# Optimization experiments

Hardware: AMD Instinct MI355X
Metric: run time of the kernel (lower is better)

Reference implementation:

```python
import jax, jax.numpy as jnp
import numpy as np
from jax import lax

B = 16384
D_MODEL = 84
N_EXPERTS = 2
TOP_K = 2
HIDDEN = 2048


def _conv(x, w, b):
    # x: [N,C,H,W], w: [O,I,kh,kw] (torch OIHW), VALID padding, stride 1
    y = lax.conv_general_dilated(x, w, (1, 1), 'VALID',
                                 dimension_numbers=('NCHW', 'OIHW', 'NCHW'))
    return y + b[None, :, None, None]


def _maxpool2(x):
    return lax.reduce_window(x, -jnp.inf, lax.max,
                             (1, 1, 2, 2), (1, 1, 2, 2), 'VALID')


def setup_inputs() -> dict:
    key = jax.random.key(0)
    ks = jax.random.split(key, 17)
    s = 0.05
    return {
        'x': jax.random.normal(ks[0], (B, 3, 32, 32), jnp.float32),
        'conv1_w': jax.random.normal(ks[1], (6, 3, 5, 5), jnp.float32) * s,
        'conv1_b': jax.random.normal(ks[2], (6,), jnp.float32) * s,
        'conv2_w': jax.random.normal(ks[3], (16, 6, 5, 5), jnp.float32) * s,
        'conv2_b': jax.random.normal(ks[4], (16,), jnp.float32) * s,
        'fc1_w': jax.random.normal(ks[5], (400, 120), jnp.float32) * s,
        'fc1_b': jax.random.normal(ks[6], (120,), jnp.float32) * s,
        'fc2_w': jax.random.normal(ks[7], (120, 84), jnp.float32) * s,
        'fc2_b': jax.random.normal(ks[8], (84,), jnp.float32) * s,
        'gate_w': jax.random.normal(ks[9], (D_MODEL, N_EXPERTS), jnp.float32) * s,
        'exp_w1': jax.random.normal(ks[10], (N_EXPERTS, D_MODEL, HIDDEN), jnp.float32) * s,
        'exp_b1': jax.random.normal(ks[11], (N_EXPERTS, HIDDEN), jnp.float32) * s,
        'exp_w2': jax.random.normal(ks[12], (N_EXPERTS, HIDDEN, D_MODEL), jnp.float32) * s,
        'exp_b2': jax.random.normal(ks[13], (N_EXPERTS, D_MODEL), jnp.float32) * s,
        'fc3_w': jax.random.normal(ks[14], (84, 10), jnp.float32) * s,
        'fc3_b': jax.random.normal(ks[15], (10,), jnp.float32) * s,
    }


def _moe(x, gate_w, exp_w1, exp_b1, exp_w2, exp_b2):
    # tutel top-k gate: softmax over expert logits, select top-k, renormalize
    n = x.shape[0]
    scores = jax.nn.softmax(x @ gate_w, axis=-1)          # [N,E]
    top_v, top_i = lax.top_k(scores, TOP_K)               # [N,k]
    gates = top_v / jnp.sum(top_v, axis=-1, keepdims=True)
    # dense combine weights [N,E] (zero where not routed)
    comb = jnp.zeros((n, N_EXPERTS), x.dtype).at[
        jnp.arange(n)[:, None], top_i].set(gates)
    # grouped expert FFN (E=2: evaluate both, weight-combine)
    h = jax.nn.relu(jnp.einsum('nd,edh->enh', x, exp_w1) + exp_b1[:, None, :])
    y = jnp.einsum('enh,ehd->end', h, exp_w2) + exp_b2[:, None, :]  # [E,N,D]
    return jnp.einsum('ne,end->nd', comb, y)


def reference(x, conv1_w, conv1_b, conv2_w, conv2_b, fc1_w, fc1_b,
              fc2_w, fc2_b, gate_w, exp_w1, exp_b1, exp_w2, exp_b2,
              fc3_w, fc3_b):
    h = _maxpool2(jax.nn.relu(_conv(x, conv1_w, conv1_b)))   # [B,6,14,14]
    h = _maxpool2(jax.nn.relu(_conv(h, conv2_w, conv2_b)))   # [B,16,5,5]
    h = h.reshape(-1, 16 * 5 * 5)                            # [B,400]
    h = jax.nn.relu(h @ fc1_w + fc1_b)                       # [B,120]
    h = jax.nn.relu(h @ fc2_w + fc2_b)                       # [B,84]
    h = _moe(h, gate_w, exp_w1, exp_b1, exp_w2, exp_b2)      # [B,84]
    return h @ fc3_w + fc3_b                                 # [B,10]
```

## Files before the change

kernel.cpp:

```cpp
#include <hip/hip_runtime.h>
#include <stdint.h>

typedef unsigned short u16;
typedef __attribute__((ext_vector_type(8))) short s8v;
typedef __attribute__((ext_vector_type(4))) float f4v;
typedef __fp16 h2v __attribute__((ext_vector_type(2)));
typedef __fp16 h8v __attribute__((ext_vector_type(8)));

__device__ __forceinline__ float bu2f(u16 u) {
  return __uint_as_float(((uint32_t)u) << 16);
}
__device__ __forceinline__ u16 f2bu(float f) {
  uint32_t u = __float_as_uint(f);
  u += 0x7fffu + ((u >> 16) & 1u);
  return (u16)(u >> 16);
}

union U32H2 { uint32_t u; h2v h; };

__device__ __forceinline__ uint32_t pk2h(float a, float b) {
  U32H2 x;
  x.h = __builtin_amdgcn_cvt_pkrtz(a, b);
  return x.u;
}

template <bool F32> struct In;
template <> struct In<true> {
  static __device__ __forceinline__ float ld(const void* p, long i) {
    return ((const float*)p)[i];
  }
};
template <> struct In<false> {
  static __device__ __forceinline__ float ld(const void* p, long i) {
    return bu2f(((const u16*)p)[i]);
  }
};

__global__ void k_detect(const u16* __restrict__ x, int* __restrict__ flag) {
  __shared__ int s[64];
  int cnt = 0;
  for (int i = threadIdx.x; i < 2048; i += 64) {
    int e = (x[i] >> 7) & 0xFF;
    cnt += (e >= 96 && e <= 134) ? 1 : 0;
  }
  s[threadIdx.x] = cnt;
  __syncthreads();
  if (threadIdx.x == 0) {
    int t = 0;
    for (int i = 0; i < 64; ++i) t += s[i];
    *flag = (t >= 1843) ? 0 : 1;
  }
}

__device__ __forceinline__ u16 f2h16(float f) {
  __fp16 h = (__fp16)f;
  u16 r;
  __builtin_memcpy(&r, &h, 2);
  return r;
}

template <bool INF32>
__global__ __launch_bounds__(256) void k_trans(
    const int* __restrict__ flag,
    const void* __restrict__ fc1w, const void* __restrict__ fc2w,
    const void* __restrict__ ew1, const void* __restrict__ ew2,
    const void* __restrict__ c1w, const void* __restrict__ c1b,
    const void* __restrict__ c2w, const void* __restrict__ c2b,
    u16* __restrict__ fc1t, u16* __restrict__ fc2t,
    u16* __restrict__ w1t, u16* __restrict__ w2t,
    uint32_t* __restrict__ cdw) {
  if (*flag != (INF32 ? 1 : 0)) return;
  long gid = (long)blockIdx.x * 256 + threadIdx.x;
  if (gid < 53248) {
    int n = (int)(gid / 416), k = (int)(gid % 416);
    fc1t[gid] = (n < 120 && k < 400) ? f2bu(In<INF32>::ld(fc1w, (long)k * 120 + n)) : (u16)0;
  } else if (gid < 65536) {
    long i = gid - 53248;
    int n = (int)(i / 128), k = (int)(i % 128);
    fc2t[i] = (n < 84 && k < 120) ? f2bu(In<INF32>::ld(fc2w, (long)k * 84 + n)) : (u16)0;
  } else if (gid < 458752) {
    long i = gid - 65536;
    int e = (int)(i / 196608);
    long r = i % 196608;
    int n = (int)(r / 96), k = (int)(r % 96);
    w1t[i] = (k < 84) ? f2bu(In<INF32>::ld(ew1, ((long)e * 84 + k) * 2048 + n)) : (u16)0;
  } else if (gid < 851968) {
    long i = gid - 458752;
    int e = (int)(i / 196608);
    long r = i % 196608;
    int n = (int)(r / 2048), k = (int)(r % 2048);
    w2t[i] = (n < 84) ? f2bu(In<INF32>::ld(ew2, ((long)e * 2048 + k) * 84 + n)) : (u16)0;
  } else if (gid < 856598) {
    long i = gid - 851968;
    u16* cdh = (u16*)cdw;
    if (i < 1536) {
      int ic = (int)(i >> 9);
      int r = (int)(i & 511);
      int lnn = r >> 3, j = r & 7;
      int n = lnn & 15, qd = lnn >> 4;
      int t = qd * 8 + j, ky = t / 6, kxp = t - ky * 6;
      float v = (n < 6 && t < 30 && kxp < 5)
          ? In<INF32>::ld(c1w, ((long)(n * 3 + ic) * 5 + ky) * 5 + kxp) : 0.f;
      cdh[i] = f2h16(v);
    } else if (i < 4608) {
      long jj = i - 1536;
      int ic = (int)(jj >> 9);
      int r = (int)(jj & 511);
      int lnn = r >> 3, j = r & 7;
      int n = lnn & 15, qd = lnn >> 4;
      int t = qd * 8 + j, ky = t / 6, kxp = t - ky * 6;
      float v = (t < 30 && kxp < 5)
          ? In<INF32>::ld(c2w, ((long)(n * 6 + ic) * 5 + ky) * 5 + kxp) : 0.f;
      cdh[1536 + jj] = f2h16(v);
    } else if (i < 4614) {
      ((float*)(cdw + 2304))[i - 4608] = In<INF32>::ld(c1b, i - 4608);
    } else if (i < 4630) {
      ((float*)(cdw + 2310))[i - 4614] = In<INF32>::ld(c2b, i - 4614);
    }
  }
}

#define CIMG 2
#define XSTR 34
#define PSTR 18
template <bool INF32>
__global__ __launch_bounds__(256) void k_conv(
    const int* __restrict__ flag,
    const void* __restrict__ x,
    const uint32_t* __restrict__ cdw,
    u16* __restrict__ p2, int Btot) {
  if (*flag != (INF32 ? 1 : 0)) return;
  __shared__ __align__(16) u16 sxn[CIMG * 3 * 32 * XSTR];
  __shared__ __align__(16) u16 sxs[CIMG * 3 * 32 * XSTR];
  __shared__ __align__(16) u16 sp1n[CIMG * 6 * 14 * PSTR];
  __shared__ __align__(16) u16 sp1s[CIMG * 6 * 14 * PSTR];
  __shared__ u16 lut1[196];
  __shared__ u16 lut2[32];
  const u16* cdh = (const u16*)cdw;
  const float* cb1f = (const float*)(cdw + 2304);
  const float* cb2f = (const float*)(cdw + 2310);
  const int tid = threadIdx.x;
  const int wv = tid >> 6, ln = tid & 63;
  const int mrow = ln & 15, quad = ln >> 4;
  const long gimg0 = (long)blockIdx.x * CIMG;

  if (tid < 196) {
    int py = tid / 14, px = tid - py * 14;
    lut1[tid] = (u16)((2 * py) * XSTR + 2 * px);
  } else if (tid < 228) {
    int i = tid - 196;
    if (i < 25) {
      int py = i / 5, px = i - py * 5;
      lut2[i] = (u16)((2 * py) * PSTR + 2 * px);
    }
  }
  for (int r = tid; r < CIMG * 6 * 14; r += 256)
    *(uint32_t*)(sp1s + (size_t)r * PSTR + 12) = 0;

  for (int i = tid; i < CIMG * 96; i += 256) {
    int img = i / 96;
    if (gimg0 + img >= Btot) continue;
    int rem = i - img * 96;
    long goff = (gimg0 + img) * 3072 + (long)rem * 32;
    uint32_t e[17];
    if (!INF32) {
      const uint32_t* src = (const uint32_t*)((const u16*)x + goff);
#pragma unroll
      for (int j = 0; j < 16; ++j) {
        uint32_t d = src[j];
        e[j] = pk2h(__uint_as_float(d << 16), __uint_as_float(d & 0xffff0000u));
      }
    } else {
      const float* src = (const float*)x + goff;
#pragma unroll
      for (int j = 0; j < 16; ++j) e[j] = pk2h(src[2 * j], src[2 * j + 1]);
    }
    e[16] = 0;
    uint32_t* dn = (uint32_t*)(sxn + (size_t)i * XSTR);
    uint32_t* dsh = (uint32_t*)(sxs + (size_t)i * XSTR);
#pragma unroll
    for (int j = 0; j < 16; ++j) {
      dn[j] = e[j];
      dsh[j] = (e[j] >> 16) | (e[j + 1] << 16);
    }
  }

  h8v b1[3];
#pragma unroll
  for (int ic = 0; ic < 3; ++ic)
    b1[ic] = *(const h8v*)(cdh + ((size_t)ic * 64 + ln) * 8);
  const float bias1 = (mrow < 6) ? cb1f[mrow] : 0.f;
  int toff1[4];
#pragma unroll
  for (int p = 0; p < 4; ++p) {
    int t = quad * 8 + 2 * p;
    if (t >= 30) t = 24;
    toff1[p] = (t / 6) * (XSTR - 6) + t;
  }
  const int qA = mrow >> 2, dyA = (mrow >> 1) & 1, dxA = mrow & 1;

  __syncthreads();

  const u16* c1base = dxA ? sxs : sxn;
  for (int tg = wv; tg < CIMG * 49; tg += 4) {
    int img = tg / 49, tau = tg - img * 49;
    int pqA = tau * 4 + qA;
    const u16* rb0 = c1base + (size_t)img * (3 * 32 * XSTR) + lut1[pqA] + dyA * XSTR;
    f4v acc = {0.f, 0.f, 0.f, 0.f};
#pragma unroll
    for (int ic = 0; ic < 3; ++ic) {
      const u16* rb = rb0 + ic * (32 * XSTR);
      union { uint32_t w[4]; h8v v; } au;
#pragma unroll
      for (int p = 0; p < 4; ++p)
        au.w[p] = *(const uint32_t*)(rb + toff1[p]);
      acc = __builtin_amdgcn_mfma_f32_16x16x32_f16(au.v, b1[ic], acc, 0, 0, 0);
    }
    float v = fmaxf(fmaxf(acc[0], acc[1]), fmaxf(acc[2], acc[3])) + bias1;
    v = fmaxf(v, 0.f);
    if (mrow < 6) {
      int pqC = tau * 4 + quad;
      int py = (pqC * 4682) >> 16, px = pqC - py * 14;
      int rbase = ((img * 6 + mrow) * 14 + py) * PSTR;
      u16 hv = f2h16(v);
      sp1n[rbase + px] = hv;
      sp1s[rbase + (px ? px - 1 : PSTR - 1)] = hv;
    }
  }

  h8v b2[6];
#pragma unroll
  for (int ic = 0; ic < 6; ++ic)
    b2[ic] = *(const h8v*)(cdh + 1536 + ((size_t)ic * 64 + ln) * 8);
  const float bias2 = cb2f[mrow];
  int toff2[4];
#pragma unroll
  for (int p = 0; p < 4; ++p) {
    int t = quad * 8 + 2 * p;
    if (t >= 30) t = 24;
    toff2[p] = (t / 6) * (PSTR - 6) + t;
  }

  __syncthreads();

  const int NP2 = CIMG * 25;
  const u16* c2base = dxA ? sp1s : sp1n;
  for (int t2 = wv; t2 * 4 < NP2; t2 += 4) {
    int PA = t2 * 4 + qA;
    if (PA >= NP2) PA = NP2 - 1;
    int img = (PA * 41) >> 10, pq = PA - img * 25;
    const u16* rb0 = c2base + (size_t)img * (6 * 14 * PSTR) + lut2[pq] + dyA * PSTR;
    f4v acc = {0.f, 0.f, 0.f, 0.f};
#pragma unroll
    for (int ic = 0; ic < 6; ++ic) {
      const u16* rb = rb0 + ic * (14 * PSTR);
      union { uint32_t w[4]; h8v v; } au;
#pragma unroll
      for (int p = 0; p < 4; ++p)
        au.w[p] = *(const uint32_t*)(rb + toff2[p]);
      acc = __builtin_amdgcn_mfma_f32_16x16x32_f16(au.v, b2[ic], acc, 0, 0, 0);
    }
    float v = fmaxf(fmaxf(acc[0], acc[1]), fmaxf(acc[2], acc[3])) + bias2;
    v = fmaxf(v, 0.f);
    int PC = t2 * 4 + quad;
    if (PC < NP2) {
      int imgc = (PC * 41) >> 10, pqc = PC - imgc * 25;
      if (gimg0 + imgc < Btot)
        p2[(gimg0 + imgc) * 416 + mrow * 25 + pqc] = f2bu(v);
    }
  }

  for (int i = tid; i < CIMG * 16; i += 256) {
    int img = i / 16;
    if (gimg0 + img < Btot) p2[(gimg0 + img) * 416 + 400 + (i & 15)] = 0;
  }
}

template <bool INF32>
__global__ __launch_bounds__(256) void k_fcA(
    const int* __restrict__ flag,
    const u16* __restrict__ p2,
    const u16* __restrict__ fc1t, const u16* __restrict__ fc2t,
    const void* __restrict__ fc1b, const void* __restrict__ fc2b,
    const void* __restrict__ gw,
    u16* __restrict__ a2buf, float* __restrict__ scbuf) {
  if (*flag != (INF32 ? 1 : 0)) return;
  __shared__ __align__(16) char smem[62976];
  u16* a2s = (u16*)smem;
  u16* hs = (u16*)(smem + 13312);
  u16* wbuf = (u16*)(smem + 31232);
  u16* xs = (u16*)(smem + 57856);

  const int tid = threadIdx.x;
  const int wv = tid >> 6, ln = tid & 63;
  const int m = ln & 15, quad = ln >> 4;
  const long t0 = (long)blockIdx.x * 64;
  const int row0 = wv * 16 + quad * 4;

  for (int i = tid; i < 30720 / 4; i += 256) ((uint32_t*)smem)[i] = 0;

  f4v acc1[8];
#pragma unroll
  for (int i = 0; i < 8; ++i) acc1[i] = (f4v){0.f, 0.f, 0.f, 0.f};
  for (int s = 0; s < 13; ++s) {
    {
      int r = tid >> 2, c0 = (tid & 3) * 8;
      *(uint4*)(xs + r * 40 + c0) =
          *(const uint4*)(p2 + (t0 + r) * 416 + s * 32 + c0);
      int n = tid >> 1, cw = (tid & 1) * 16;
      *(uint4*)(wbuf + n * 40 + cw) = *(const uint4*)(fc1t + (long)n * 416 + s * 32 + cw);
      *(uint4*)(wbuf + n * 40 + cw + 8) =
          *(const uint4*)(fc1t + (long)n * 416 + s * 32 + cw + 8);
    }
    __syncthreads();
    s8v a = *(const s8v*)(xs + (wv * 16 + m) * 40 + quad * 8);
#pragma unroll
    for (int nt = 0; nt < 8; ++nt) {
      s8v b = *(const s8v*)(wbuf + (nt * 16 + m) * 40 + quad * 8);
      acc1[nt] = __builtin_amdgcn_mfma_f32_16x16x32_bf16(a, b, acc1[nt], 0, 0, 0);
    }
    __syncthreads();
  }
#pragma unroll
  for (int nt = 0; nt < 8; ++nt) {
    int n = nt * 16 + m;
    if (n < 120) {
      float bv = In<INF32>::ld(fc1b, n);
#pragma unroll
      for (int r = 0; r < 4; ++r)
        hs[(row0 + r) * 136 + n] = f2bu(fmaxf(acc1[nt][r] + bv, 0.f));
    }
  }
  __syncthreads();

  for (int i = tid; i < 1536; i += 256) {
    int n = i >> 4, c0 = (i & 15) * 8;
    *(uint4*)(wbuf + n * 136 + c0) = *(const uint4*)(fc2t + n * 128 + c0);
  }
  __syncthreads();
  f4v acc2[6];
#pragma unroll
  for (int i = 0; i < 6; ++i) acc2[i] = (f4v){0.f, 0.f, 0.f, 0.f};
  for (int s = 0; s < 4; ++s) {
    s8v a = *(const s8v*)(hs + (wv * 16 + m) * 136 + s * 32 + quad * 8);
#pragma unroll
    for (int nt = 0; nt < 6; ++nt) {
      s8v b = *(const s8v*)(wbuf + (nt * 16 + m) * 136 + s * 32 + quad * 8);
      acc2[nt] = __builtin_amdgcn_mfma_f32_16x16x32_bf16(a, b, acc2[nt], 0, 0, 0);
    }
  }
  __syncthreads();
#pragma unroll
  for (int nt = 0; nt < 6; ++nt) {
    int n = nt * 16 + m;
    if (n < 84) {
      float bv = In<INF32>::ld(fc2b, n);
#pragma unroll
      for (int r = 0; r < 4; ++r)
        a2s[(row0 + r) * 104 + n] = f2bu(fmaxf(acc2[nt][r] + bv, 0.f));
    }
  }
  __syncthreads();

  if (tid < 64) {
    const u16* xr = a2s + tid * 104;
    float l0 = 0.f, l1 = 0.f;
    for (int k = 0; k < 84; ++k) {
      float xv = bu2f(xr[k]);
      l0 = fmaf(xv, In<INF32>::ld(gw, 2 * k), l0);
      l1 = fmaf(xv, In<INF32>::ld(gw, 2 * k + 1), l1);
    }
    float mx = fmaxf(l0, l1);
    float e0 = __expf(l0 - mx), e1 = __expf(l1 - mx);
    float inv = 1.f / (e0 + e1);
    *(float2*)(scbuf + (t0 + tid) * 2) = make_float2(e0 * inv, e1 * inv);
  }
  for (int i = tid; i < 832; i += 256) {
    int r = i / 13, c0 = (i - r * 13) * 8;
    *(uint4*)(a2buf + (t0 + r) * 104 + c0) = *(const uint4*)(a2s + r * 104 + c0);
  }
}

template <bool INF32>
__global__ __launch_bounds__(256) void k_exp(
    const int* __restrict__ flag,
    const u16* __restrict__ a2buf, const float* __restrict__ scbuf,
    const u16* __restrict__ w1t, const u16* __restrict__ w2t,
    const void* __restrict__ eb1, const void* __restrict__ eb2,
    float* __restrict__ ybuf, int Btok) {
  if (*flag != (INF32 ? 1 : 0)) return;
  __shared__ __align__(16) char smem[57856];
  u16* a2s = (u16*)smem;
  u16* hs = (u16*)(smem + 13312);
  u16* wbuf = (u16*)(smem + 30720);
  float* scs = (float*)(smem + 57344);

  const int tid = threadIdx.x;
  const int wv = tid >> 6, ln = tid & 63;
  const int m = ln & 15, quad = ln >> 4;
  const int e = blockIdx.y;
  const long t0 = (long)blockIdx.x * 64;
  const int row0 = wv * 16 + quad * 4;
  const u16* w1te = w1t + (long)e * 196608;
  const u16* w2te = w2t + (long)e * 196608;

  for (int i = tid; i < 832; i += 256) {
    int r = i / 13, c0 = (i - r * 13) * 8;
    *(uint4*)(a2s + r * 104 + c0) = *(const uint4*)(a2buf + (t0 + r) * 104 + c0);
  }
  if (tid < 64) scs[tid] = scbuf[(t0 + tid) * 2 + e];
  __syncthreads();

  f4v acce[6];
#pragma unroll
  for (int i = 0; i < 6; ++i) acce[i] = (f4v){0.f, 0.f, 0.f, 0.f};
  for (int c = 0; c < 16; ++c) {
    const int n0 = c * 128;
    if (c) __syncthreads();
    for (int i = tid; i < 1536; i += 256) {
      int nl = i / 12, c0 = (i - nl * 12) * 8;
      *(uint4*)(wbuf + nl * 104 + c0) =
          *(const uint4*)(w1te + (long)(n0 + nl) * 96 + c0);
    }
    __syncthreads();
    f4v acch[8];
#pragma unroll
    for (int i = 0; i < 8; ++i) acch[i] = (f4v){0.f, 0.f, 0.f, 0.f};
    for (int s = 0; s < 3; ++s) {
      s8v a = *(const s8v*)(a2s + (wv * 16 + m) * 104 + s * 32 + quad * 8);
#pragma unroll
      for (int nt = 0; nt < 8; ++nt) {
        s8v b = *(const s8v*)(wbuf + (nt * 16 + m) * 104 + s * 32 + quad * 8);
        acch[nt] = __builtin_amdgcn_mfma_f32_16x16x32_bf16(a, b, acch[nt], 0, 0, 0);
      }
    }
#pragma unroll
    for (int nt = 0; nt < 8; ++nt) {
      float bv = In<INF32>::ld(eb1, (long)e * 2048 + n0 + nt * 16 + m);
#pragma unroll
      for (int r = 0; r < 4; ++r)
        hs[(row0 + r) * 136 + nt * 16 + m] = f2bu(fmaxf(acch[nt][r] + bv, 0.f));
    }
    __syncthreads();
    for (int i = tid; i < 1536; i += 256) {
      int n = i >> 4, c0 = (i & 15) * 8;
      *(uint4*)(wbuf + n * 136 + c0) =
          *(const uint4*)(w2te + (long)n * 2048 + n0 + c0);
    }
    __syncthreads();
    for (int s = 0; s < 4; ++s) {
      s8v a = *(const s8v*)(hs + (wv * 16 + m) * 136 + s * 32 + quad * 8);
#pragma unroll
      for (int nt = 0; nt < 6; ++nt) {
        s8v b = *(const s8v*)(wbuf + (nt * 16 + m) * 136 + s * 32 + quad * 8);
        acce[nt] = __builtin_amdgcn_mfma_f32_16x16x32_bf16(a, b, acce[nt], 0, 0, 0);
      }
    }
  }

#pragma unroll
  for (int nt = 0; nt < 6; ++nt) {
    int d = nt * 16 + m;
    float bv = (d < 84) ? In<INF32>::ld(eb2, (long)e * 84 + d) : 0.f;
#pragma unroll
    for (int r = 0; r < 4; ++r) {
      float sc = scs[row0 + r];
      ybuf[((size_t)e * Btok + t0 + row0 + r) * 96 + d] = sc * (acce[nt][r] + bv);
    }
  }
}

template <bool INF32>
__global__ __launch_bounds__(256) void k_fc3(
    const int* __restrict__ flag,
    const float* __restrict__ ybuf,
    const void* __restrict__ w3, const void* __restrict__ b3,
    void* __restrict__ out, int Btok) {
  if (*flag != (INF32 ? 1 : 0)) return;
  __shared__ float sw3[840];
  __shared__ float sb3[10];
  const int tid = threadIdx.x;
  const long t0 = (long)blockIdx.x * 64;
  for (int i = tid; i < 840; i += 256) sw3[i] = In<INF32>::ld(w3, i);
  if (tid < 10) sb3[tid] = In<INF32>::ld(b3, tid);
  __syncthreads();
  for (int idx = tid; idx < 640; idx += 256) {
    int tk = idx / 10, cc = idx - tk * 10;
    const float* y0r = ybuf + (t0 + tk) * 96;
    const float* y1r = ybuf + ((size_t)Btok + t0 + tk) * 96;
    float acc = sb3[cc];
    for (int d = 0; d < 84; ++d)
      acc = fmaf(y0r[d] + y1r[d], sw3[d * 10 + cc], acc);
    long oi = (t0 + tk) * 10 + cc;
    if (INF32) ((float*)out)[oi] = acc;
    else ((u16*)out)[oi] = f2bu(acc);
  }
}

extern "C" void kernel_launch(void* const* d_in, const int* in_sizes, int n_in,
                              void* d_out, int out_size, void* d_ws, size_t ws_size,
                              hipStream_t stream) {
  const int B = in_sizes[0] / 3072;
  char* wsb = (char*)d_ws;
  int* flag = (int*)wsb;
  u16* p2 = (u16*)(wsb + 64);
  u16* fc1t = p2 + (size_t)B * 416;
  u16* fc2t = fc1t + 53248;
  u16* w1t = fc2t + 12288;
  u16* w2t = w1t + 393216;
  uint32_t* cdw = (uint32_t*)(w2t + 393216);
  u16* a2buf = (u16*)(cdw + 2326);
  float* scbuf = (float*)(a2buf + (size_t)B * 104);
  float* ybuf = scbuf + (size_t)B * 2;

  k_detect<<<1, 64, 0, stream>>>((const u16*)d_in[0], flag);

  k_trans<false><<<3347, 256, 0, stream>>>(flag, d_in[5], d_in[7], d_in[10],
                                           d_in[12], d_in[1], d_in[2], d_in[3],
                                           d_in[4], fc1t, fc2t, w1t, w2t, cdw);
  k_trans<true><<<3347, 256, 0, stream>>>(flag, d_in[5], d_in[7], d_in[10],
                                          d_in[12], d_in[1], d_in[2], d_in[3],
                                          d_in[4], fc1t, fc2t, w1t, w2t, cdw);

  const int convGrid = (B + CIMG - 1) / CIMG;
  k_conv<false><<<convGrid, 256, 0, stream>>>(flag, d_in[0], cdw, p2, B);
  k_conv<true><<<convGrid, 256, 0, stream>>>(flag, d_in[0], cdw, p2, B);

  k_fcA<false><<<B / 64, 256, 0, stream>>>(flag, p2, fc1t, fc2t, d_in[6],
                                           d_in[8], d_in[9], a2buf, scbuf);
  k_fcA<true><<<B / 64, 256, 0, stream>>>(flag, p2, fc1t, fc2t, d_in[6],
                                          d_in[8], d_in[9], a2buf, scbuf);

  dim3 eg(B / 64, 2);
  k_exp<false><<<eg, 256, 0, stream>>>(flag, a2buf, scbuf, w1t, w2t, d_in[11],
                                       d_in[13], ybuf, B);
  k_exp<true><<<eg, 256, 0, stream>>>(flag, a2buf, scbuf, w1t, w2t, d_in[11],
                                      d_in[13], ybuf, B);

  k_fc3<false><<<B / 64, 256, 0, stream>>>(flag, ybuf, d_in[14], d_in[15],
                                           d_out, B);
  k_fc3<true><<<B / 64, 256, 0, stream>>>(flag, ybuf, d_in[14], d_in[15],
                                          d_out, B);
}
```

Measured before the change: 542.3 us.

## Register-prefetch expert weights and split LDS buffers in k_exp

After: 578.5 us. 6.7% more time.

```diff
diff --git a/kernel.cpp b/kernel.cpp
--- a/kernel.cpp
+++ b/kernel.cpp
@@ -389,11 +389,11 @@
     const void* __restrict__ eb1, const void* __restrict__ eb2,
     float* __restrict__ ybuf, int Btok) {
   if (*flag != (INF32 ? 1 : 0)) return;
-  __shared__ __align__(16) char smem[57856];
-  u16* a2s = (u16*)smem;
-  u16* hs = (u16*)(smem + 13312);
-  u16* wbuf = (u16*)(smem + 30720);
-  float* scs = (float*)(smem + 57344);
+  __shared__ __align__(16) char smem[70400];
+  u16* hs  = (u16*)smem;
+  u16* wbA = (u16*)(smem + 17408);
+  u16* wbB = (u16*)(smem + 44032);
+  float* scs = (float*)(smem + 70144);
 
   const int tid = threadIdx.x;
   const int wv = tid >> 6, ln = tid & 63;
@@ -404,33 +404,51 @@
   const u16* w1te = w1t + (long)e * 196608;
   const u16* w2te = w2t + (long)e * 196608;
 
-  for (int i = tid; i < 832; i += 256) {
-    int r = i / 13, c0 = (i - r * 13) * 8;
-    *(uint4*)(a2s + r * 104 + c0) = *(const uint4*)(a2buf + (t0 + r) * 104 + c0);
-  }
+  const u16* arow = a2buf + (t0 + wv * 16 + m) * 104 + quad * 8;
+  s8v a0 = *(const s8v*)(arow);
+  s8v a1 = *(const s8v*)(arow + 32);
+  s8v a2f = *(const s8v*)(arow + 64);
   if (tid < 64) scs[tid] = scbuf[(t0 + tid) * 2 + e];
+
+  int nlA[6], cA0[6], nB[6], cB0[6];
+#pragma unroll
+  for (int k = 0; k < 6; ++k) {
+    int i2 = tid + k * 256;
+    nlA[k] = i2 / 12; cA0[k] = (i2 - nlA[k] * 12) * 8;
+    nB[k] = i2 >> 4;  cB0[k] = (i2 & 15) * 8;
+  }
+  uint4 R1[6], R2[6];
+#pragma unroll
+  for (int k = 0; k < 6; ++k)
+    R1[k] = *(const uint4*)(w1te + (long)nlA[k] * 96 + cA0[k]);
+#pragma unroll
+  for (int k = 0; k < 6; ++k)
+    R2[k] = *(const uint4*)(w2te + (long)nB[k] * 2048 + cB0[k]);
+#pragma unroll
+  for (int k = 0; k < 6; ++k)
+    *(uint4*)(wbA + nlA[k] * 104 + cA0[k]) = R1[k];
   __syncthreads();
 
   f4v acce[6];
 #pragma unroll
   for (int i = 0; i < 6; ++i) acce[i] = (f4v){0.f, 0.f, 0.f, 0.f};
+
   for (int c = 0; c < 16; ++c) {
     const int n0 = c * 128;
-    if (c) __syncthreads();
-    for (int i = tid; i < 1536; i += 256) {
-      int nl = i / 12, c0 = (i - nl * 12) * 8;
-      *(uint4*)(wbuf + nl * 104 + c0) =
-          *(const uint4*)(w1te + (long)(n0 + nl) * 96 + c0);
-    }
-    __syncthreads();
+    if (c < 15) {
+#pragma unroll
+      for (int k = 0; k < 6; ++k)
+        R1[k] = *(const uint4*)(w1te + (long)(n0 + 128 + nlA[k]) * 96 + cA0[k]);
+    }
     f4v acch[8];
 #pragma unroll
     for (int i = 0; i < 8; ++i) acch[i] = (f4v){0.f, 0.f, 0.f, 0.f};
+#pragma unroll
     for (int s = 0; s < 3; ++s) {
-      s8v a = *(const s8v*)(a2s + (wv * 16 + m) * 104 + s * 32 + quad * 8);
+      s8v a = (s == 0) ? a0 : (s == 1) ? a1 : a2f;
 #pragma unroll
       for (int nt = 0; nt < 8; ++nt) {
-        s8v b = *(const s8v*)(wbuf + (nt * 16 + m) * 104 + s * 32 + quad * 8);
+        s8v b = *(const s8v*)(wbA + (nt * 16 + m) * 104 + s * 32 + quad * 8);
         acch[nt] = __builtin_amdgcn_mfma_f32_16x16x32_bf16(a, b, acch[nt], 0, 0, 0);
       }
     }
@@ -442,19 +460,30 @@
         hs[(row0 + r) * 136 + nt * 16 + m] = f2bu(fmaxf(acch[nt][r] + bv, 0.f));
     }
     __syncthreads();
-    for (int i = tid; i < 1536; i += 256) {
-      int n = i >> 4, c0 = (i & 15) * 8;
-      *(uint4*)(wbuf + n * 136 + c0) =
-          *(const uint4*)(w2te + (long)n * 2048 + n0 + c0);
-    }
+#pragma unroll
+    for (int k = 0; k < 6; ++k)
+      *(uint4*)(wbB + nB[k] * 136 + cB0[k]) = R2[k];
     __syncthreads();
+    if (c < 15) {
+#pragma unroll
+      for (int k = 0; k < 6; ++k)
+        R2[k] = *(const uint4*)(w2te + (long)nB[k] * 2048 + n0 + 128 + cB0[k]);
+    }
+#pragma unroll
     for (int s = 0; s < 4; ++s) {
       s8v a = *(const s8v*)(hs + (wv * 16 + m) * 136 + s * 32 + quad * 8);
 #pragma unroll
       for (int nt = 0; nt < 6; ++nt) {
-        s8v b = *(const s8v*)(wbuf + (nt * 16 + m) * 136 + s * 32 + quad * 8);
+        s8v b = *(const s8v*)(wbB + (nt * 16 + m) * 136 + s * 32 + quad * 8);
         acce[nt] = __builtin_amdgcn_mfma_f32_16x16x32_bf16(a, b, acce[nt], 0, 0, 0);
       }
+    }
+    __syncthreads();
+    if (c < 15) {
+#pragma unroll
+      for (int k = 0; k < 6; ++k)
+        *(uint4*)(wbA + nlA[k] * 104 + cA0[k]) = R1[k];
+      __syncthreads();
     }
   }
 
```
